# Performance work log

Hardware: AMD Instinct MI355X
Metric: run time of the kernel (lower is better)

Reference implementation:

```python
import jax, jax.numpy as jnp
import numpy as np
import math

D_MODEL, N_HEADS, D_FF = 512, 8, 2048
B, S = 4, 2048
EPS = 1e-6


def _layernorm(x, alpha, bias):
    # Faithful to the torch module: std is unbiased (ddof=1) and eps is added to std, not var.
    m = jnp.mean(x, axis=-1, keepdims=True)
    s = jnp.std(x, axis=-1, keepdims=True, ddof=1)
    return alpha * (x - m) / (s + EPS) + bias


def setup_inputs() -> dict:
    key = jax.random.key(0)
    ks = jax.random.split(key, 16)
    d, f = D_MODEL, D_FF
    sd = 1.0 / math.sqrt(d)
    sf = 1.0 / math.sqrt(f)
    return {
        "x": jax.random.normal(ks[0], (B, S, d), jnp.float32),
        "wq": jax.random.normal(ks[1], (d, d), jnp.float32) * sd,
        "bq": jnp.zeros((d,), jnp.float32),
        "wk": jax.random.normal(ks[2], (d, d), jnp.float32) * sd,
        "bk": jnp.zeros((d,), jnp.float32),
        "wv": jax.random.normal(ks[3], (d, d), jnp.float32) * sd,
        "bv": jnp.zeros((d,), jnp.float32),
        "wo": jax.random.normal(ks[4], (d, d), jnp.float32) * sd,
        "bo": jnp.zeros((d,), jnp.float32),
        "w1": jax.random.normal(ks[5], (d, f), jnp.float32) * sd,
        "b1": jnp.zeros((f,), jnp.float32),
        "w2": jax.random.normal(ks[6], (f, d), jnp.float32) * sf,
        "b2": jnp.zeros((d,), jnp.float32),
        "ln1_a": jnp.ones((d,), jnp.float32),
        "ln1_b": jnp.zeros((d,), jnp.float32),
        "ln2_a": jnp.ones((d,), jnp.float32),
        "ln2_b": jnp.zeros((d,), jnp.float32),
    }


def reference(x, wq, bq, wk, bk, wv, bv, wo, bo, w1, b1, w2, b2, ln1_a, ln1_b, ln2_a, ln2_b):
    b, s, d = x.shape
    h, dk = N_HEADS, d // N_HEADS
    # QKV projections -> [b, h, s, dk]
    q = (x @ wq + bq).reshape(b, s, h, dk).transpose(0, 2, 1, 3)
    k = (x @ wk + bk).reshape(b, s, h, dk).transpose(0, 2, 1, 3)
    v = (x @ wv + bv).reshape(b, s, h, dk).transpose(0, 2, 1, 3)
    # Manual scaled-dot-product attention (no mask in EncoderBlock path)
    scores = jnp.einsum("bhqd,bhkd->bhqk", q, k) / jnp.sqrt(jnp.float32(dk))
    probs = jax.nn.softmax(scores, axis=-1)
    attn = jnp.einsum("bhqk,bhkd->bhqd", probs, v)
    concat = attn.transpose(0, 2, 1, 3).reshape(b, s, d)
    mha_out = concat @ wo + bo
    # Residual + LayerNorm 1
    y = _layernorm(x + mha_out, ln1_a, ln1_b)
    # FFN + Residual + LayerNorm 2
    ff = jax.nn.relu(y @ w1 + b1) @ w2 + b2
    return _layernorm(y + ff, ln2_a, ln2_b)
```

## Files before the change

### kernel.cpp

```cpp
#include <hip/hip_runtime.h>
#include <hip/hip_bf16.h>


typedef __bf16 bf16;
typedef __bf16 bf16x4 __attribute__((ext_vector_type(4)));
typedef __bf16 bf16x8 __attribute__((ext_vector_type(8)));
typedef float  f32x4  __attribute__((ext_vector_type(4)));

#define NBATCH 4
#define SEQ    2048
#define DMODEL 512
#define NHEADS 8
#define DHEAD  64
#define DFF    2048
#define MTOT   (NBATCH * SEQ)
#define WS_NEED 73416704u
#define QSCALE (0.125f * 1.44269504f)

__device__ __forceinline__ f32x4 mfma16(bf16x8 a, bf16x8 b, f32x4 c) {
    return __builtin_amdgcn_mfma_f32_16x16x32_bf16(a, b, c, 0, 0, 0);
}

__device__ __forceinline__ void lds16(const bf16* g, bf16* l) {
    __builtin_amdgcn_global_load_lds(
        (const __attribute__((address_space(1))) void*)g,
        (__attribute__((address_space(3))) void*)l, 16, 0, 0);
}

__device__ __forceinline__ float scrub(float f) {
    return (fabsf(f) < 1e30f) ? f : 0.f;
}

__device__ __forceinline__ void xcd_swizzle(int BMv, int BNv, int& mb, int& nb) {
    int gx = gridDim.x, gy = gridDim.y;
    int lin = blockIdx.y * gx + blockIdx.x;
    int q = (gx * gy) >> 3;
    lin = (lin & 7) * q + (lin >> 3);
    int mbi = lin / gy, nbi = lin - mbi * gy;
    mb = mbi * BMv; nb = nbi * BNv;
}

__global__ void sentinel_kernel(bf16* out) {
    out[threadIdx.x] = (bf16)1000.0f;
}

__global__ __launch_bounds__(256) void prep_kernel(
        const float* x,
        const float* wq, const float* wk, const float* wv, const float* wo,
        const float* w1, const float* w2,
        const float* bq, const float* bk, const float* bv, const float* bo,
        const float* b1, const float* b2,
        const float* l1a, const float* l1b, const float* l2a, const float* l2b,
        bf16* __restrict__ xcv,
        bf16* __restrict__ wT, bf16* __restrict__ w1T, bf16* __restrict__ w2T,
        bf16* __restrict__ prm) {
    __shared__ bf16 tile[32][33];
    int b = blockIdx.x;
    if (b < 4096) {
        int i = (b * 256 + threadIdx.x) * 4;
        float4 f = *(const float4*)(x + i);
        bf16x4 o = {(bf16)scrub(f.x), (bf16)scrub(f.y),
                    (bf16)scrub(f.z), (bf16)scrub(f.w)};
        *(bf16x4*)(xcv + i) = o;
        return;
    }
    if (b < 4106) {
        int pb = b - 4096;
        const float* srcs[10] = {bq, bk, bv, bo, b1, b2, l1a, l1b, l2a, l2b};
        const int len[10] = {512,512,512,512,2048,512,512,512,512,512};
        const int dst[10] = {0,512,1024,1536,2048,4096,4608,5120,5632,6144};
        const float* s = srcs[pb];
        bf16* d = prm + dst[pb];
        for (int i = threadIdx.x; i < len[pb]; i += 256)
            d[i] = (bf16)scrub(s[i]);
        return;
    }
    const float* in; bf16* out; int K, N, bx, by;
    if (b < 5130) {
        int idx = b - 4106, z = idx >> 8, rem = idx & 255;
        const float* srcs[4] = {wq, wk, wv, wo};
        in = srcs[z]; out = wT + (size_t)z * 262144;
        K = 512; N = 512; bx = rem & 15; by = rem >> 4;
    } else if (b < 6154) {
        int idx = b - 5130;
        in = w1; out = w1T; K = 512; N = 2048; bx = idx & 63; by = idx >> 6;
    } else {
        int idx = b - 6154;
        in = w2; out = w2T; K = 2048; N = 512; bx = idx & 15; by = idx >> 4;
    }
    int tx = threadIdx.x & 31, ty = threadIdx.x >> 5;
    int n0 = bx * 32, k0 = by * 32;
#pragma unroll
    for (int i = 0; i < 4; i++) {
        int kl = ty * 4 + i;
        tile[kl][tx] = (bf16)scrub(in[(size_t)(k0 + kl) * N + n0 + tx]);
    }
    __syncthreads();
#pragma unroll
    for (int i = 0; i < 4; i++) {
        int nl = ty * 4 + i;
        out[(size_t)(n0 + nl) * K + k0 + tx] = tile[tx][nl];
    }
}

template <bool RELU>
__global__ __launch_bounds__(512) void gemm256(
        const bf16* __restrict__ A, const bf16* __restrict__ BT,
        const bf16* __restrict__ bias, bf16* __restrict__ Cout,
        int M, int N, int K) {
    __shared__ __align__(16) bf16 Abuf[2][256 * 64];
    __shared__ __align__(16) bf16 Bbuf[2][256 * 64];

    int tid  = threadIdx.x;
    int w    = tid >> 6, lane = tid & 63;
    int quad = lane >> 4, l15 = lane & 15;
    int mb, nb;
    xcd_swizzle(256, 256, mb, nb);
    int wm = (w >> 2) * 128, wn = (w & 3) * 64;

    int srow   = lane >> 3;
    int gchunk = ((lane & 7) ^ srow) << 3;
    int rb0    = w * 32;
    int sw     = l15 & 7;

    f32x4 acc[8][4] = {};
    int NT = K >> 6;

#define STAGE256(BUF, KO)                                                    \
    _Pragma("unroll")                                                        \
    for (int a = 0; a < 4; a++) {                                            \
        int rb = rb0 + a * 8;                                                \
        lds16(&A [(size_t)(mb + rb + srow) * K + (KO) + gchunk],             \
              &Abuf[BUF][rb * 64]);                                          \
        lds16(&BT[(size_t)(nb + rb + srow) * K + (KO) + gchunk],             \
              &Bbuf[BUF][rb * 64]);                                          \
    }

    STAGE256(0, 0);

    for (int k = 0; k < NT; k++) {
        if (k + 1 < NT) {
            STAGE256((k + 1) & 1, (k + 1) << 6);
            asm volatile("s_waitcnt vmcnt(8)" ::: "memory");
        } else {
            asm volatile("s_waitcnt vmcnt(0)" ::: "memory");
        }
        __builtin_amdgcn_sched_barrier(0);
        __builtin_amdgcn_s_barrier();
        __builtin_amdgcn_sched_barrier(0);

        const bf16* Ab = &Abuf[k & 1][0];
        const bf16* Bb = &Bbuf[k & 1][0];
        __builtin_amdgcn_s_setprio(1);
#pragma unroll
        for (int ks = 0; ks < 2; ks++) {
            int ch = (((ks << 2) + quad) ^ sw) << 3;
            bf16x8 bfr[4];
#pragma unroll
            for (int j = 0; j < 4; j++)
                bfr[j] = *(const bf16x8*)&Bb[(wn + j * 16 + l15) * 64 + ch];
#pragma unroll
            for (int i = 0; i < 8; i++) {
                bf16x8 af = *(const bf16x8*)&Ab[(wm + i * 16 + l15) * 64 + ch];
#pragma unroll
                for (int j = 0; j < 4; j++)
                    acc[i][j] = mfma16(af, bfr[j], acc[i][j]);
            }
        }
        __builtin_amdgcn_s_setprio(0);
        __builtin_amdgcn_sched_barrier(0);
        __builtin_amdgcn_s_barrier();
        __builtin_amdgcn_sched_barrier(0);
    }
#undef STAGE256

#pragma unroll
    for (int j = 0; j < 4; j++) {
        int n = nb + wn + j * 16 + l15;
        float bv = (float)bias[n];
#pragma unroll
        for (int i = 0; i < 8; i++) {
            int mBase = mb + wm + i * 16 + quad * 4;
#pragma unroll
            for (int r = 0; r < 4; r++) {
                float v = acc[i][j][r] + bv;
                if (RELU) v = v > 0.f ? v : 0.f;
                Cout[(size_t)(mBase + r) * N + n] = (bf16)v;
            }
        }
    }
}

template <bool RELU>
__global__ __launch_bounds__(256) void gemm_bt64(
        const bf16* __restrict__ A, const bf16* __restrict__ BT,
        const bf16* __restrict__ bias, bf16* __restrict__ Cout,
        int M, int N, int K) {
    constexpr int BM = 64, BN = 128;
    __shared__ __align__(16) bf16 As0[BM * 32], As1[BM * 32];
    __shared__ __align__(16) bf16 Bs0[BN * 32], Bs1[BN * 32];

    int tid  = threadIdx.x;
    int wid  = tid >> 6, lane = tid & 63;
    int quad = lane >> 4, l15 = lane & 15;
    int mb, nb;
    xcd_swizzle(BM, BN, mb, nb);
    int wm = (wid >> 1) * 32, wn = (wid & 1) * 64;

    f32x4 acc[2][4] = {};

    int cA = wid * 64 + lane;
    int arA = cA >> 2, acA = (cA & 3) * 8;
    int cB0 = wid * 128 + lane, cB1 = cB0 + 64;
    int br0 = cB0 >> 2, bc0 = (cB0 & 3) * 8;
    int br1 = cB1 >> 2, bc1 = (cB1 & 3) * 8;

    lds16(&A [(size_t)(mb + arA) * K + acA], &As0[wid * 512]);
    lds16(&BT[(size_t)(nb + br0) * K + bc0], &Bs0[wid * 1024]);
    lds16(&BT[(size_t)(nb + br1) * K + bc1], &Bs0[wid * 1024 + 512]);
    __syncthreads();

    for (int k0 = 0; k0 < K; k0 += 64) {
        lds16(&A [(size_t)(mb + arA) * K + k0 + 32 + acA], &As1[wid * 512]);
        lds16(&BT[(size_t)(nb + br0) * K + k0 + 32 + bc0], &Bs1[wid * 1024]);
        lds16(&BT[(size_t)(nb + br1) * K + k0 + 32 + bc1], &Bs1[wid * 1024 + 512]);
        {
            bf16x8 a0[2], b0[4];
#pragma unroll
            for (int i = 0; i < 2; i++)
                a0[i] = *(const bf16x8*)&As0[(wm + i * 16 + l15) * 32 + quad * 8];
#pragma unroll
            for (int j = 0; j < 4; j++)
                b0[j] = *(const bf16x8*)&Bs0[(wn + j * 16 + l15) * 32 + quad * 8];
#pragma unroll
            for (int i = 0; i < 2; i++)
#pragma unroll
                for (int j = 0; j < 4; j++)
                    acc[i][j] = mfma16(a0[i], b0[j], acc[i][j]);
        }
        __syncthreads();
        if (k0 + 64 < K) {
            lds16(&A [(size_t)(mb + arA) * K + k0 + 64 + acA], &As0[wid * 512]);
            lds16(&BT[(size_t)(nb + br0) * K + k0 + 64 + bc0], &Bs0[wid * 1024]);
            lds16(&BT[(size_t)(nb + br1) * K + k0 + 64 + bc1], &Bs0[wid * 1024 + 512]);
        }
        {
            bf16x8 a1[2], b1[4];
#pragma unroll
            for (int i = 0; i < 2; i++)
                a1[i] = *(const bf16x8*)&As1[(wm + i * 16 + l15) * 32 + quad * 8];
#pragma unroll
            for (int j = 0; j < 4; j++)
                b1[j] = *(const bf16x8*)&Bs1[(wn + j * 16 + l15) * 32 + quad * 8];
#pragma unroll
            for (int i = 0; i < 2; i++)
#pragma unroll
                for (int j = 0; j < 4; j++)
                    acc[i][j] = mfma16(a1[i], b1[j], acc[i][j]);
        }
        __syncthreads();
    }

#pragma unroll
    for (int j = 0; j < 4; j++) {
        int n = nb + wn + j * 16 + l15;
        float bv = (float)bias[n];
#pragma unroll
        for (int i = 0; i < 2; i++) {
            int mBase = mb + wm + i * 16 + quad * 4;
#pragma unroll
            for (int r = 0; r < 4; r++) {
                float v = acc[i][j][r] + bv;
                if (RELU) v = v > 0.f ? v : 0.f;
                Cout[(size_t)(mBase + r) * N + n] = (bf16)v;
            }
        }
    }
}

__global__ __launch_bounds__(256) void gemm_qkv(
        const bf16* __restrict__ A, const bf16* __restrict__ BT,
        const bf16* __restrict__ bias,
        bf16* __restrict__ Cq, bf16* __restrict__ Ck, bf16* __restrict__ Cv,
        int M, int N, int K) {
    constexpr int BM = 128, BN = 128;
    __shared__ __align__(16) bf16 As0[BM * 32], As1[BM * 32];
    __shared__ __align__(16) bf16 Bs0[BN * 32], Bs1[BN * 32];
    __shared__ __align__(16) bf16 Ts[128 * 136];

    int tid  = threadIdx.x;
    int wid  = tid >> 6, lane = tid & 63;
    int quad = lane >> 4, l15 = lane & 15;
    int mb, nb;
    xcd_swizzle(BM, BN, mb, nb);
    int wm = (wid >> 1) * 64, wn = (wid & 1) * 64;

    f32x4 acc[4][4] = {};

    int c0 = wid * 128 + lane, c1 = c0 + 64;
    int ar0 = c0 >> 2, ac0 = (c0 & 3) * 8;
    int ar1 = c1 >> 2, ac1 = (c1 & 3) * 8;
    int o0 = wid * 1024, o1 = wid * 1024 + 512;

    lds16(&A [(size_t)(mb + ar0) * K + ac0], &As0[o0]);
    lds16(&A [(size_t)(mb + ar1) * K + ac1], &As0[o1]);
    lds16(&BT[(size_t)(nb + ar0) * K + ac0], &Bs0[o0]);
    lds16(&BT[(size_t)(nb + ar1) * K + ac1], &Bs0[o1]);
    __syncthreads();

    for (int k0 = 0; k0 < K; k0 += 64) {
        lds16(&A [(size_t)(mb + ar0) * K + k0 + 32 + ac0], &As1[o0]);
        lds16(&A [(size_t)(mb + ar1) * K + k0 + 32 + ac1], &As1[o1]);
        lds16(&BT[(size_t)(nb + ar0) * K + k0 + 32 + ac0], &Bs1[o0]);
        lds16(&BT[(size_t)(nb + ar1) * K + k0 + 32 + ac1], &Bs1[o1]);
        {
            bf16x8 af[4], bfr[4];
#pragma unroll
            for (int i = 0; i < 4; i++)
                af[i] = *(const bf16x8*)&As0[(wm + i * 16 + l15) * 32 + quad * 8];
#pragma unroll
            for (int j = 0; j < 4; j++)
                bfr[j] = *(const bf16x8*)&Bs0[(wn + j * 16 + l15) * 32 + quad * 8];
#pragma unroll
            for (int i = 0; i < 4; i++)
#pragma unroll
                for (int j = 0; j < 4; j++)
                    acc[i][j] = mfma16(af[i], bfr[j], acc[i][j]);
        }
        __syncthreads();
        if (k0 + 64 < K) {
            lds16(&A [(size_t)(mb + ar0) * K + k0 + 64 + ac0], &As0[o0]);
            lds16(&A [(size_t)(mb + ar1) * K + k0 + 64 + ac1], &As0[o1]);
            lds16(&BT[(size_t)(nb + ar0) * K + k0 + 64 + ac0], &Bs0[o0]);
            lds16(&BT[(size_t)(nb + ar1) * K + k0 + 64 + ac1], &Bs0[o1]);
        }
        {
            bf16x8 af[4], bfr[4];
#pragma unroll
            for (int i = 0; i < 4; i++)
                af[i] = *(const bf16x8*)&As1[(wm + i * 16 + l15) * 32 + quad * 8];
#pragma unroll
            for (int j = 0; j < 4; j++)
                bfr[j] = *(const bf16x8*)&Bs1[(wn + j * 16 + l15) * 32 + quad * 8];
#pragma unroll
            for (int i = 0; i < 4; i++)
#pragma unroll
                for (int j = 0; j < 4; j++)
                    acc[i][j] = mfma16(af[i], bfr[j], acc[i][j]);
        }
        __syncthreads();
    }

    int reg = nb >> 9;
    if (reg < 2) {
        bf16* C = reg ? Ck : Cq;
        float scl = reg ? 1.0f : QSCALE;
#pragma unroll
        for (int j = 0; j < 4; j++) {
            int n = nb + wn + j * 16 + l15;
            float bv = (float)bias[n];
            int nn = n & 511;
            int h = nn >> 6, dk = nn & 63;
#pragma unroll
            for (int i = 0; i < 4; i++) {
                int mBase = mb + wm + i * 16 + quad * 4;
#pragma unroll
                for (int r = 0; r < 4; r++) {
                    float v = (acc[i][j][r] + bv) * scl;
                    int m = mBase + r;
                    int b = m >> 11, s = m & (SEQ - 1);
                    C[((size_t)(b * NHEADS + h) * SEQ + s) * DHEAD + dk] = (bf16)v;
                }
            }
        }
    } else {
#pragma unroll
        for (int j = 0; j < 4; j++) {
            int nl = wn + j * 16 + l15;
            float bv = (float)bias[nb + nl];
#pragma unroll
            for (int i = 0; i < 4; i++) {
                int ml = wm + i * 16 + quad * 4;
                bf16x4 pk;
#pragma unroll
                for (int r = 0; r < 4; r++) pk[r] = (bf16)(acc[i][j][r] + bv);
                *(bf16x4*)&Ts[nl * 136 + ml] = pk;
            }
        }
        __syncthreads();
        int nl = tid >> 1, half = tid & 1;
        int nn = (nb + nl) & 511;
        int h = nn >> 6, dk = nn & 63;
        int bb = mb >> 11, s0 = mb & (SEQ - 1);
        bf16* dst = &Cv[((size_t)(bb * NHEADS + h) * DHEAD + dk) * SEQ + s0 + half * 64];
        const bf16* srcl = &Ts[nl * 136 + half * 64];
#pragma unroll
        for (int v = 0; v < 8; v++)
            *(uint4*)(dst + v * 8) = *(const uint4*)(srcl + v * 8);
    }
}

__global__ __launch_bounds__(256) void attn_kernel(
        const bf16* __restrict__ Q, const bf16* __restrict__ K,
        const bf16* __restrict__ VT, bf16* __restrict__ Out) {
    __shared__ __align__(16) bf16 Ks[2][64 * 64];
    __shared__ __align__(16) bf16 Vs[2][64 * 64];
    __shared__ __align__(16) bf16 Pb[4][16 * 64];
    int tid  = threadIdx.x;
    int wid  = tid >> 6, lane = tid & 63;
    int quad = lane >> 4, l15 = lane & 15;

    int lin = blockIdx.y * 16 + blockIdx.x;
    lin = (lin & 7) * 64 + (lin >> 3);
    int bh = lin >> 4;
    int qb = (lin & 15) * 128 + wid * 32;

    const bf16* Qh = Q  + (size_t)bh * SEQ * DHEAD;
    const bf16* Kh = K  + (size_t)bh * SEQ * DHEAD;
    const bf16* Vh = VT + (size_t)bh * DHEAD * SEQ;

    bf16x8 bQ0[2], bQ1[2];
#pragma unroll
    for (int c = 0; c < 2; c++) {
        const bf16* qp = &Qh[(qb + c * 16 + l15) * DHEAD + quad * 8];
        bQ0[c] = *(const bf16x8*)qp;
        bQ1[c] = *(const bf16x8*)(qp + 32);
    }

    bf16x8 vONE;
#pragma unroll
    for (int i = 0; i < 8; i++) vONE[i] = (bf16)1.0f;

    int srow = lane >> 3;
    int scol = ((lane & 7) ^ srow) << 3;
    int ldsb = wid * 1024;
    int krA = wid * 16 + srow, krB = krA + 8;

    int r7q = l15 & 7;
    int e0 = ((quad ^ r7q) << 3);
    int e1 = e0 ^ 32;

    f32x4 lacc[2] = {};
    f32x4 Oacc[2][4] = {};

    lds16(&Kh[(size_t)krA * DHEAD + scol], &Ks[0][ldsb]);
    lds16(&Kh[(size_t)krB * DHEAD + scol], &Ks[0][ldsb + 512]);
    lds16(&Vh[(size_t)krA * SEQ + scol],   &Vs[0][ldsb]);
    lds16(&Vh[(size_t)krB * SEQ + scol],   &Vs[0][ldsb + 512]);
    __syncthreads();

#define ATTN_STEP(CUR, NXT, KB, PF)                                          \
    {                                                                        \
        if (PF) {                                                            \
            lds16(&Kh[(size_t)((KB) + krA) * DHEAD + scol], &Ks[NXT][ldsb]); \
            lds16(&Kh[(size_t)((KB) + krB) * DHEAD + scol],                  \
                  &Ks[NXT][ldsb + 512]);                                     \
            lds16(&Vh[(size_t)krA * SEQ + (KB) + scol], &Vs[NXT][ldsb]);     \
            lds16(&Vh[(size_t)krB * SEQ + (KB) + scol],                      \
                  &Vs[NXT][ldsb + 512]);                                     \
        }                                                                    \
        bf16x8 aK0[4], aK1[4], bV0[4], bV1[4];                               \
        _Pragma("unroll")                                                    \
        for (int t = 0; t < 4; t++) {                                        \
            const bf16* kp = &Ks[CUR][(t * 16 + l15) * 64];                  \
            aK0[t] = *(const bf16x8*)(kp + e0);                              \
            aK1[t] = *(const bf16x8*)(kp + e1);                              \
            const bf16* vp = &Vs[CUR][(t * 16 + l15) * 64];                  \
            bV0[t] = *(const bf16x8*)(vp + e0);                              \
            bV1[t] = *(const bf16x8*)(vp + e1);                              \
        }                                                                    \
        _Pragma("unroll")                                                    \
        for (int c = 0; c < 2; c++) {                                        \
            __builtin_amdgcn_s_setprio(1);                                   \
            f32x4 st[4];                                                     \
            _Pragma("unroll")                                                \
            for (int t = 0; t < 4; t++) {                                    \
                f32x4 zv = {0.f, 0.f, 0.f, 0.f};                             \
                st[t] = mfma16(aK1[t], bQ1[c], mfma16(aK0[t], bQ0[c], zv));  \
            }                                                                \
            bf16* myP = Pb[wid];                                             \
            _Pragma("unroll")                                                \
            for (int t = 0; t < 4; t++) {                                    \
                bf16x4 pk;                                                   \
                _Pragma("unroll")                                            \
                for (int r = 0; r < 4; r++)                                  \
                    pk[r] = (bf16)__builtin_amdgcn_exp2f(                    \
                                fminf(st[t][r], 60.f));                      \
                int pch = ((2 * t + (quad >> 1)) ^ r7q) << 3;                \
                *(bf16x4*)&myP[l15 * 64 + pch + ((quad & 1) << 2)] = pk;     \
            }                                                                \
            bf16x8 aP0 = *(const bf16x8*)&myP[l15 * 64 + e0];                \
            bf16x8 aP1 = *(const bf16x8*)&myP[l15 * 64 + e1];                \
            _Pragma("unroll")                                                \
            for (int nt = 0; nt < 4; nt++)                                   \
                Oacc[c][nt] = mfma16(aP1, bV1[nt],                           \
                                     mfma16(aP0, bV0[nt], Oacc[c][nt]));     \
            lacc[c] = mfma16(aP1, vONE, mfma16(aP0, vONE, lacc[c]));         \
            __builtin_amdgcn_s_setprio(0);                                   \
        }                                                                    \
        __syncthreads();                                                     \
    }

    for (int it2 = 0; it2 < SEQ / 128; it2++) {
        ATTN_STEP(0, 1, (2 * it2 + 1) * 64, true);
        ATTN_STEP(1, 0, (2 * it2 + 2) * 64, (it2 + 1 < SEQ / 128));
    }
#undef ATTN_STEP

    int b = bh >> 3, hd = bh & 7;
#pragma unroll
    for (int c = 0; c < 2; c++) {
        float linv[4];
#pragma unroll
        for (int r = 0; r < 4; r++)
            linv[r] = 1.f / lacc[c][r];
#pragma unroll
        for (int nt = 0; nt < 4; nt++)
#pragma unroll
            for (int r = 0; r < 4; r++) {
                int s = qb + c * 16 + quad * 4 + r;
                Out[((size_t)(b * SEQ + s)) * DMODEL + hd * 64 + nt * 16 + l15]
                    = (bf16)(Oacc[c][nt][r] * linv[r]);
            }
    }
}

__global__ __launch_bounds__(256) void ln_kernel(
        const bf16* __restrict__ X, const bf16* __restrict__ T,
        const bf16* __restrict__ Al, const bf16* __restrict__ Bl,
        void* __restrict__ Out, int final_out) {
    int wid = threadIdx.x >> 6, lane = threadIdx.x & 63;
    int row = blockIdx.x * 4 + wid;
    const bf16* xr = X + (size_t)row * DMODEL;
    const bf16* tr = T + (size_t)row * DMODEL;
    bf16x8 xv = *(const bf16x8*)&xr[lane * 8];
    bf16x8 tv = *(const bf16x8*)&tr[lane * 8];
    float v[8];
#pragma unroll
    for (int i = 0; i < 8; i++) v[i] = (float)xv[i] + (float)tv[i];
    float sum = 0.f, sq = 0.f;
#pragma unroll
    for (int i = 0; i < 8; i++) { sum += v[i]; sq += v[i] * v[i]; }
#pragma unroll
    for (int m = 1; m < 64; m <<= 1) {
        sum += __shfl_xor(sum, m);
        sq  += __shfl_xor(sq,  m);
    }
    float mean = sum * (1.f / DMODEL);
    float var  = (sq - DMODEL * mean * mean) * (1.f / (DMODEL - 1));
    var = var > 0.f ? var : 0.f;
    float inv = 1.f / (sqrtf(var) + 1e-6f);
#pragma unroll
    for (int i = 0; i < 8; i++) {
        int c = lane * 8 + i;
        float yv = (float)Al[c] * (v[i] - mean) * inv + (float)Bl[c];
        yv = fminf(fmaxf(yv, -1e4f), 1e4f);
        size_t idx = (size_t)row * DMODEL + c;
        if (final_out) ((float*)Out)[idx] = yv;
        else           ((bf16*)Out)[idx]  = (bf16)yv;
    }
}

extern "C" void kernel_launch(void* const* d_in, const int* in_sizes, int n_in,
                              void* d_out, int out_size, void* d_ws, size_t ws_size,
                              hipStream_t stream) {
    if (ws_size < WS_NEED) {
        sentinel_kernel<<<1, 64, 0, stream>>>((bf16*)d_out);
        return;
    }

    const float* x  = (const float*)d_in[0];
    const float* wq = (const float*)d_in[1],  *bq = (const float*)d_in[2];
    const float* wk = (const float*)d_in[3],  *bk = (const float*)d_in[4];
    const float* wv = (const float*)d_in[5],  *bv = (const float*)d_in[6];
    const float* wo = (const float*)d_in[7],  *bo = (const float*)d_in[8];
    const float* w1 = (const float*)d_in[9],  *b1 = (const float*)d_in[10];
    const float* w2 = (const float*)d_in[11], *b2 = (const float*)d_in[12];
    const float* ln1a = (const float*)d_in[13], *ln1b = (const float*)d_in[14];
    const float* ln2a = (const float*)d_in[15], *ln2b = (const float*)d_in[16];

    char* ws = (char*)d_ws;
    bf16* wT   = (bf16*)(ws + 0);
    bf16* woT  = (bf16*)(ws + 1572864);
    bf16* w1T  = (bf16*)(ws + 2097152);
    bf16* w2T  = (bf16*)(ws + 4194304);
    bf16* xcv  = (bf16*)(ws + 6291456);
    bf16* prm  = (bf16*)(ws + 14680064);
    bf16* regA = (bf16*)(ws + 14696448);
    bf16* regB = (bf16*)(ws + 23085056);
    bf16* regC = (bf16*)(ws + 31473664);
    bf16* ff1  = (bf16*)(ws + 39862272);
    bf16* aout = (bf16*)d_out;

    bf16 *pbq = prm, *pbo = prm + 1536;
    bf16 *pb1 = prm + 2048, *pb2 = prm + 4096;
    bf16 *pl1a = prm + 4608, *pl1b = prm + 5120;
    bf16 *pl2a = prm + 5632, *pl2b = prm + 6144;

    prep_kernel<<<7178, 256, 0, stream>>>(x, wq, wk, wv, wo, w1, w2,
                                          bq, bk, bv, bo, b1, b2,
                                          ln1a, ln1b, ln2a, ln2b,
                                          xcv, wT, w1T, w2T, prm);

    gemm_qkv<<<dim3(64, 12), 256, 0, stream>>>(xcv, wT, pbq,
                                               regA, regB, regC,
                                               MTOT, 3 * DMODEL, DMODEL);

    attn_kernel<<<dim3(SEQ / 128, NBATCH * NHEADS), 256, 0, stream>>>(
        regA, regB, regC, aout);

    gemm_bt64<false><<<dim3(128, 4), 256, 0, stream>>>(aout, woT, pbo, regA,
                                                       MTOT, DMODEL, DMODEL);

    ln_kernel<<<MTOT / 4, 256, 0, stream>>>(xcv, regA, pl1a, pl1b, regB, 0);

    gemm256<true><<<dim3(32, 8), 512, 0, stream>>>(regB, w1T, pb1, ff1,
                                                   MTOT, DFF, DMODEL);

    gemm_bt64<false><<<dim3(128, 4), 256, 0, stream>>>(ff1, w2T, pb2, regA,
                                                       MTOT, DMODEL, DFF);

    ln_kernel<<<MTOT / 4, 256, 0, stream>>>(regB, regA, pl2a, pl2b, d_out, 1);
}
```

Baseline: 278.9 us.

## Split-K the output projection and FFN2 GEMMs, reducing partials in layernorm

Replaces the 64x128 GEMM used for the output projection and the second FFN matmul with a two-way split-K variant that writes fp32 partial sums to separate buffers. The residual layernorm kernel now sums the input, both partials and the bias-included first partial before normalising. This doubles the number of blocks to improve CU utilisation and shortens each block's K loop. In exchange it writes and reads larger fp32 intermediates and reuses workspace and output buffers for partials.

```diff
diff --git a/kernel.cpp b/kernel.cpp
--- a/kernel.cpp
+++ b/kernel.cpp
@@ -191,10 +191,11 @@
     }
 }
 
-template <bool RELU>
-__global__ __launch_bounds__(256) void gemm_bt64(
+__global__ __launch_bounds__(256) void gemm_sk(
         const bf16* __restrict__ A, const bf16* __restrict__ BT,
-        const bf16* __restrict__ bias, bf16* __restrict__ Cout,
+        const bf16* __restrict__ bias,
+        float* __restrict__ P1, float* __restrict__ P2a,
+        float* __restrict__ P2b,
         int M, int N, int K) {
     constexpr int BM = 64, BN = 128;
     __shared__ __align__(16) bf16 As0[BM * 32], As1[BM * 32];
@@ -206,6 +207,8 @@
     int mb, nb;
     xcd_swizzle(BM, BN, mb, nb);
     int wm = (wid >> 1) * 32, wn = (wid & 1) * 64;
+    int kp = blockIdx.z;
+    int kbase = kp * (K >> 1), kend = kbase + (K >> 1);
 
     f32x4 acc[2][4] = {};
 
@@ -215,12 +218,12 @@
     int br0 = cB0 >> 2, bc0 = (cB0 & 3) * 8;
     int br1 = cB1 >> 2, bc1 = (cB1 & 3) * 8;
 
-    lds16(&A [(size_t)(mb + arA) * K + acA], &As0[wid * 512]);
-    lds16(&BT[(size_t)(nb + br0) * K + bc0], &Bs0[wid * 1024]);
-    lds16(&BT[(size_t)(nb + br1) * K + bc1], &Bs0[wid * 1024 + 512]);
+    lds16(&A [(size_t)(mb + arA) * K + kbase + acA], &As0[wid * 512]);
+    lds16(&BT[(size_t)(nb + br0) * K + kbase + bc0], &Bs0[wid * 1024]);
+    lds16(&BT[(size_t)(nb + br1) * K + kbase + bc1], &Bs0[wid * 1024 + 512]);
     __syncthreads();
 
-    for (int k0 = 0; k0 < K; k0 += 64) {
+    for (int k0 = kbase; k0 < kend; k0 += 64) {
         lds16(&A [(size_t)(mb + arA) * K + k0 + 32 + acA], &As1[wid * 512]);
         lds16(&BT[(size_t)(nb + br0) * K + k0 + 32 + bc0], &Bs1[wid * 1024]);
         lds16(&BT[(size_t)(nb + br1) * K + k0 + 32 + bc1], &Bs1[wid * 1024 + 512]);
@@ -239,7 +242,7 @@
                     acc[i][j] = mfma16(a0[i], b0[j], acc[i][j]);
         }
         __syncthreads();
-        if (k0 + 64 < K) {
+        if (k0 + 64 < kend) {
             lds16(&A [(size_t)(mb + arA) * K + k0 + 64 + acA], &As0[wid * 512]);
             lds16(&BT[(size_t)(nb + br0) * K + k0 + 64 + bc0], &Bs0[wid * 1024]);
             lds16(&BT[(size_t)(nb + br1) * K + k0 + 64 + bc1], &Bs0[wid * 1024 + 512]);
@@ -264,15 +267,21 @@
 #pragma unroll
     for (int j = 0; j < 4; j++) {
         int n = nb + wn + j * 16 + l15;
-        float bv = (float)bias[n];
+        float bv = kp ? 0.f : (float)bias[n];
 #pragma unroll
         for (int i = 0; i < 2; i++) {
             int mBase = mb + wm + i * 16 + quad * 4;
 #pragma unroll
             for (int r = 0; r < 4; r++) {
+                int row = mBase + r;
                 float v = acc[i][j][r] + bv;
-                if (RELU) v = v > 0.f ? v : 0.f;
-                Cout[(size_t)(mBase + r) * N + n] = (bf16)v;
+                if (kp == 0) {
+                    P1[(size_t)row * N + n] = v;
+                } else if (row < 4096) {
+                    P2a[(size_t)row * N + n] = v;
+                } else {
+                    P2b[(size_t)(row - 4096) * N + n] = v;
+                }
             }
         }
     }
@@ -525,19 +534,27 @@
     }
 }
 
-__global__ __launch_bounds__(256) void ln_kernel(
-        const bf16* __restrict__ X, const bf16* __restrict__ T,
+__global__ __launch_bounds__(256) void lnsk_kernel(
+        const bf16* __restrict__ X, const float* P1,
+        const float* __restrict__ P2a, const float* __restrict__ P2b,
         const bf16* __restrict__ Al, const bf16* __restrict__ Bl,
-        void* __restrict__ Out, int final_out) {
+        void* Out, int final_out) {
     int wid = threadIdx.x >> 6, lane = threadIdx.x & 63;
     int row = blockIdx.x * 4 + wid;
-    const bf16* xr = X + (size_t)row * DMODEL;
-    const bf16* tr = T + (size_t)row * DMODEL;
+    const bf16*  xr = X  + (size_t)row * DMODEL;
+    const float* p1 = P1 + (size_t)row * DMODEL;
+    const float* p2 = (row < 4096) ? P2a + (size_t)row * DMODEL
+                                   : P2b + (size_t)(row - 4096) * DMODEL;
     bf16x8 xv = *(const bf16x8*)&xr[lane * 8];
-    bf16x8 tv = *(const bf16x8*)&tr[lane * 8];
-    float v[8];
-#pragma unroll
-    for (int i = 0; i < 8; i++) v[i] = (float)xv[i] + (float)tv[i];
+    float4 a0 = *(const float4*)&p1[lane * 8];
+    float4 a1 = *(const float4*)&p1[lane * 8 + 4];
+    float4 c0 = *(const float4*)&p2[lane * 8];
+    float4 c1 = *(const float4*)&p2[lane * 8 + 4];
+    float v[8] = {
+        (float)xv[0] + a0.x + c0.x, (float)xv[1] + a0.y + c0.y,
+        (float)xv[2] + a0.z + c0.z, (float)xv[3] + a0.w + c0.w,
+        (float)xv[4] + a1.x + c1.x, (float)xv[5] + a1.y + c1.y,
+        (float)xv[6] + a1.z + c1.z, (float)xv[7] + a1.w + c1.w};
     float sum = 0.f, sq = 0.f;
 #pragma unroll
     for (int i = 0; i < 8; i++) { sum += v[i]; sq += v[i] * v[i]; }
@@ -592,6 +609,12 @@
     bf16* ff1  = (bf16*)(ws + 39862272);
     bf16* aout = (bf16*)d_out;
 
+    float* oP1 = (float*)(ws + 39862272);
+    float* oP2 = oP1 + 4194304;
+    float* fP1  = (float*)d_out;
+    float* fP2a = (float*)regA;
+    float* fP2b = (float*)regC;
+
     bf16 *pbq = prm, *pbo = prm + 1536;
     bf16 *pb1 = prm + 2048, *pb2 = prm + 4096;
     bf16 *pl1a = prm + 4608, *pl1b = prm + 5120;
@@ -609,16 +632,19 @@
     attn_kernel<<<dim3(SEQ / 128, NBATCH * NHEADS), 256, 0, stream>>>(
         regA, regB, regC, aout);
 
-    gemm_bt64<false><<<dim3(128, 4), 256, 0, stream>>>(aout, woT, pbo, regA,
-                                                       MTOT, DMODEL, DMODEL);
-
-    ln_kernel<<<MTOT / 4, 256, 0, stream>>>(xcv, regA, pl1a, pl1b, regB, 0);
+    gemm_sk<<<dim3(128, 4, 2), 256, 0, stream>>>(
+        aout, woT, pbo, oP1, oP2, oP2 + (size_t)4096 * DMODEL,
+        MTOT, DMODEL, DMODEL);
+
+    lnsk_kernel<<<MTOT / 4, 256, 0, stream>>>(
+        xcv, oP1, oP2, oP2 + (size_t)4096 * DMODEL, pl1a, pl1b, regB, 0);
 
     gemm256<true><<<dim3(32, 8), 512, 0, stream>>>(regB, w1T, pb1, ff1,
                                                    MTOT, DFF, DMODEL);
 
-    gemm_bt64<false><<<dim3(128, 4), 256, 0, stream>>>(ff1, w2T, pb2, regA,
-                                                       MTOT, DMODEL, DFF);
-
-    ln_kernel<<<MTOT / 4, 256, 0, stream>>>(regB, regA, pl2a, pl2b, d_out, 1);
-}
+    gemm_sk<<<dim3(128, 4, 2), 256, 0, stream>>>(
+        ff1, w2T, pb2, fP1, fP2a, fP2b, MTOT, DMODEL, DFF);
+
+    lnsk_kernel<<<MTOT / 4, 256, 0, stream>>>(
+        regB, fP1, fP2a, fP2b, pl2a, pl2b, d_out, 1);
+}
```

Result: slower. 287.4 us (+3.0%).
